# Kernel optimization log

Measured on AMD Instinct MI355X. Metric: run time of the kernel, lower is better.

The kernel has to match this reference:

```python
import jax, jax.numpy as jnp
import numpy as np

B, N = 4, 512
NZ = 95
BOX = 25.0                      # Angstrom box for random coords
CUTOFF = 15.0
SMOOTH_ON = 12.0                # cutoff * (1 - 0.2)
SMOOTH_OFF = 15.0
A1, A2, S6, S8 = 0.4145, 4.8593, 1.0, 1.2177
K1, K3 = 16.0, 4.0              # standard DFT-D3 CN / gaussian-weight constants
BOHR = 1.8897261258369282       # Angstrom -> Bohr
H2EV = 27.211386245988          # Hartree -> eV


def setup_inputs() -> dict:
    key = jax.random.key(0)
    k = jax.random.split(key, 6)
    coord = jax.random.uniform(k[0], (B, N, 3), jnp.float32) * BOX
    numbers = jax.random.randint(k[1], (B, N), 0, 86).astype(jnp.int64)
    rcov = jax.random.uniform(k[2], (NZ,), jnp.float32) * 2.0 + 1.0      # Bohr
    r4r2 = jax.random.uniform(k[3], (NZ,), jnp.float32) * 3.0 + 2.0      # a.u.
    c6ab = jax.random.uniform(k[4], (NZ, NZ, 5, 5), jnp.float32) * 20.0 + 1.0
    cn_ref = jax.random.uniform(k[5], (NZ, NZ, 5, 5), jnp.float32) * 4.0
    return dict(coord=coord, numbers=numbers, rcov=rcov, r4r2=r4r2,
                c6ab=c6ab, cn_ref=cn_ref)


def _d3_energy(coord, rcov, r4r2, c6ab, cn_ref, numbers):
    z = numbers
    # pairwise distances [B,N,N] (Angstrom), self-pairs masked
    diff = coord[:, :, None, :] - coord[:, None, :, :]
    r2 = (diff * diff).sum(-1)
    eye = jnp.eye(N, dtype=bool)[None]
    r2_safe = jnp.where(eye, 1.0, r2)
    r_ang = jnp.sqrt(r2_safe)
    pair_mask = (~eye) & (r_ang <= CUTOFF)
    r = r_ang * BOHR  # Bohr

    # coordination numbers: CN_i = sum_j 1/(1+exp(-k1*(rcov_ij/r - 1)))
    rc = rcov[z]                                   # [B,N]
    rco = rc[:, :, None] + rc[:, None, :]          # [B,N,N]
    cn_pair = jnp.where(pair_mask,
                        1.0 / (1.0 + jnp.exp(-K1 * (rco / r - 1.0))), 0.0)
    cn = cn_pair.sum(-1)                           # [B,N]

    # C6 interpolation over 5x5 reference-CN grid (gather-heavy)
    zi = z[:, :, None]   # [B,N,1]
    zj = z[:, None, :]   # [B,1,N]
    c6_ref = c6ab[zi, zj]                               # [B,N,N,5,5]
    cni_ref = cn_ref[zi, zj]                            # ref CN of atom i
    cnj_ref = jnp.swapaxes(cn_ref[zj, zi], -1, -2)      # ref CN of atom j
    dcn_i = cn[:, :, None, None, None] - cni_ref
    dcn_j = cn[:, None, :, None, None] - cnj_ref
    w = jnp.where(c6_ref > 0.0,
                  jnp.exp(-K3 * (dcn_i * dcn_i + dcn_j * dcn_j)), 0.0)
    wsum = w.sum((-1, -2))
    c6 = (c6_ref * w).sum((-1, -2)) / (wsum + 1e-20)    # [B,N,N]

    # C8 and BJ damping radius
    rr = r4r2[z]
    r4r2ij = rr[:, :, None] * rr[:, None, :]
    c8 = 3.0 * c6 * r4r2ij
    r0 = jnp.sqrt(3.0 * r4r2ij)     # sqrt(C8/C6)
    f = A1 * r0 + A2

    r6 = r2_safe * BOHR * BOHR
    r6 = r6 * r6 * r6               # r^6 in Bohr
    r8 = r6 * r * r
    e_pair = S6 * c6 / (r6 + f ** 6) + S8 * c8 / (r8 + f ** 8)

    # cutoff smoothing (smoothstep from SMOOTH_ON to SMOOTH_OFF, in Angstrom)
    x = jnp.clip((r_ang - SMOOTH_ON) / (SMOOTH_OFF - SMOOTH_ON), 0.0, 1.0)
    sw = 1.0 - x * x * (3.0 - 2.0 * x)
    e_pair = jnp.where(pair_mask, e_pair * sw, 0.0)

    # each pair counted twice in the dense matrix -> 0.5 factor; Hartree->eV
    return -0.5 * e_pair.sum((1, 2)) * H2EV   # [B]


def reference(coord, numbers, rcov, r4r2, c6ab, cn_ref):
    return _d3_energy(coord, rcov, r4r2, c6ab, cn_ref, numbers)
```

## Files before the change

kernel.cpp:

```cpp
#include <hip/hip_runtime.h>

#define NA   512
#define NB   4
#define NZT  95

#define FUSED_ELEMS (NZT * NZT * 25)
#define FUSED_BYTES (FUSED_ELEMS * 16)
#define FUSE_BLOCKS ((FUSED_ELEMS + 255) / 256)

#define SORT_OFF (((FUSED_BYTES + 63) / 64) * 64)
#define ARR_B    (NB * NA * 4)
#define EBLOCKS  (NB * NA * NA / 256)

__global__ void __launch_bounds__(256) prep_kernel(
    const float* __restrict__ coord,
    const int*   __restrict__ numbers,
    const float* __restrict__ rcov,
    const float* __restrict__ r4r2,
    const float* __restrict__ c6ab,
    const float* __restrict__ cn_ref,
    float4*      __restrict__ fused,
    float*       __restrict__ xs,
    float*       __restrict__ ys,
    float*       __restrict__ zs,
    float*       __restrict__ rcs,
    float*       __restrict__ rrs,
    int*         __restrict__ zsp)
{
    const int blk = blockIdx.x;
    if (blk < NB) {
        const int b = blk;
        __shared__ int hist[NZT];
        __shared__ int offs[NZT];
        for (int t = threadIdx.x; t < NZT; t += 256) hist[t] = 0;
        __syncthreads();

        const int i0 = threadIdx.x;
        const int i1 = threadIdx.x + 256;
        const int z0 = numbers[b * NA + i0];
        const int z1 = numbers[b * NA + i1];
        atomicAdd(&hist[z0], 1);
        atomicAdd(&hist[z1], 1);
        __syncthreads();
        if (threadIdx.x == 0) {
            int s = 0;
            for (int k = 0; k < NZT; ++k) { offs[k] = s; s += hist[k]; }
        }
        __syncthreads();

        const float* cb = coord + (size_t)b * NA * 3;
        const int base = b * NA;

        const int p0 = base + atomicAdd(&offs[z0], 1);
        xs[p0]  = cb[3 * i0 + 0];
        ys[p0]  = cb[3 * i0 + 1];
        zs[p0]  = cb[3 * i0 + 2];
        rcs[p0] = rcov[z0];
        rrs[p0] = r4r2[z0];
        zsp[p0] = z0;

        const int p1 = base + atomicAdd(&offs[z1], 1);
        xs[p1]  = cb[3 * i1 + 0];
        ys[p1]  = cb[3 * i1 + 1];
        zs[p1]  = cb[3 * i1 + 2];
        rcs[p1] = rcov[z1];
        rrs[p1] = r4r2[z1];
        zsp[p1] = z1;
        return;
    }

    const int idx = (blk - NB) * 256 + threadIdx.x;
    if (idx >= FUSED_ELEMS) return;
    const int pair = idx / 25;
    const int k    = idx - pair * 25;
    const int a    = k / 5;
    const int b2   = k - a * 5;
    const int zi   = pair / NZT;
    const int zj   = pair - zi * NZT;

    const float c6 = c6ab[(size_t)pair * 25 + k];
    const float ci = cn_ref[(size_t)pair * 25 + k];
    const float cj = cn_ref[((size_t)zj * NZT + zi) * 25 + b2 * 5 + a];
    fused[idx] = make_float4(c6, ci, cj, 0.0f);
}

__global__ void __launch_bounds__(256) cn_kernel(
    const float* __restrict__ xs,
    const float* __restrict__ ys,
    const float* __restrict__ zs,
    const float* __restrict__ rcs,
    float*       __restrict__ cn)
{
    const int bi   = blockIdx.x;
    const int b    = bi >> 9;
    const int i    = bi & (NA - 1);
    const int base = b * NA;

    const float xi  = xs[base + i];
    const float yi  = ys[base + i];
    const float zi  = zs[base + i];
    const float rci = rcs[base + i];

    float acc = 0.0f;
    #pragma unroll
    for (int t = 0; t < 2; ++t) {
        const int j = threadIdx.x + t * 256;
        if (j == i) continue;
        const float dx = xi - xs[base + j];
        const float dy = yi - ys[base + j];
        const float dz = zi - zs[base + j];
        const float r2 = dx * dx + dy * dy + dz * dz;
        const float r_ang = sqrtf(r2);
        if (r_ang <= 15.0f) {
            const float rb  = r_ang * 1.8897261258369282f;
            const float rco = rci + rcs[base + j];
            acc += 1.0f / (1.0f + __expf(-16.0f * (rco / rb - 1.0f)));
        }
    }
    #pragma unroll
    for (int off = 32; off > 0; off >>= 1)
        acc += __shfl_down(acc, off, 64);

    __shared__ float red[4];
    const int wave = threadIdx.x >> 6;
    if ((threadIdx.x & 63) == 0) red[wave] = acc;
    __syncthreads();
    if (threadIdx.x == 0) cn[bi] = red[0] + red[1] + red[2] + red[3];
}

__global__ void __launch_bounds__(256) energy_kernel(
    const float*  __restrict__ xs,
    const float*  __restrict__ ys,
    const float*  __restrict__ zs,
    const float*  __restrict__ rrs,
    const int*    __restrict__ zsp,
    const float4* __restrict__ fused,
    const float*  __restrict__ cn,
    float*        __restrict__ partials)
{
    const int tid  = blockIdx.x * 256 + threadIdx.x;
    const int b    = tid >> 18;
    const int rem  = tid & (NA * NA - 1);
    const int i    = rem >> 9;
    const int j    = rem & (NA - 1);
    const int base = b * NA;

    float e = 0.0f;
    if (i != j) {
        const float dx = xs[base + i] - xs[base + j];
        const float dy = ys[base + i] - ys[base + j];
        const float dz = zs[base + i] - zs[base + j];
        const float r2 = dx * dx + dy * dy + dz * dz;
        const float r_ang = sqrtf(r2);
        if (r_ang <= 15.0f) {
            const int zi = __builtin_amdgcn_readfirstlane(zsp[base + i]);
            const int zj = zsp[base + j];
            const float cni = cn[base + i];
            const float cnj = cn[base + j];

            const float4* tp = fused + ((size_t)zi * NZT + zj) * 25;

            float wsum = 0.0f, c6w = 0.0f;
            #pragma unroll
            for (int k = 0; k < 25; ++k) {
                const float4 t = tp[k];
                const float di = cni - t.y;
                const float dj = cnj - t.z;
                float s = di * di;
                s = fmaf(dj, dj, s);
                float w = __expf(-4.0f * s);
                w = (t.x > 0.0f) ? w : 0.0f;
                wsum += w;
                c6w  = fmaf(t.x, w, c6w);
            }
            const float c6 = c6w / (wsum + 1e-20f);

            const float rrij = rrs[base + i] * rrs[base + j];
            const float c8   = 3.0f * c6 * rrij;
            const float r0   = sqrtf(3.0f * rrij);
            const float f    = 0.4145f * r0 + 4.8593f;

            const float B2  = 1.8897261258369282f * 1.8897261258369282f;
            const float r2b = r2 * B2;
            const float r6  = r2b * r2b * r2b;
            const float r8  = r6 * r2b;
            const float f2  = f * f;
            const float f6  = f2 * f2 * f2;
            const float f8  = f6 * f2;

            float ep = c6 / (r6 + f6) + 1.2177f * c8 / (r8 + f8);

            float x = (r_ang - 12.0f) * (1.0f / 3.0f);
            x = fminf(fmaxf(x, 0.0f), 1.0f);
            const float sw = 1.0f - x * x * (3.0f - 2.0f * x);
            e = ep * sw;
        }
    }

    #pragma unroll
    for (int off = 32; off > 0; off >>= 1)
        e += __shfl_down(e, off, 64);

    __shared__ float red[4];
    const int wave = threadIdx.x >> 6;
    if ((threadIdx.x & 63) == 0) red[wave] = e;
    __syncthreads();
    if (threadIdx.x == 0)
        partials[blockIdx.x] = red[0] + red[1] + red[2] + red[3];
}

__global__ void __launch_bounds__(256) reduce_kernel(
    const float* __restrict__ partials,
    float*       __restrict__ out)
{
    const int b = blockIdx.x;
    const int P = EBLOCKS / NB;
    float s = 0.0f;
    #pragma unroll
    for (int t = 0; t < P / 256; ++t)
        s += partials[b * P + threadIdx.x + t * 256];

    #pragma unroll
    for (int off = 32; off > 0; off >>= 1)
        s += __shfl_down(s, off, 64);

    __shared__ float red[4];
    const int wave = threadIdx.x >> 6;
    if ((threadIdx.x & 63) == 0) red[wave] = s;
    __syncthreads();
    if (threadIdx.x == 0) {
        const float tot = red[0] + red[1] + red[2] + red[3];
        out[b] = tot * (-0.5f * 27.211386245988f);
    }
}

extern "C" void kernel_launch(void* const* d_in, const int* in_sizes, int n_in,
                              void* d_out, int out_size, void* d_ws, size_t ws_size,
                              hipStream_t stream) {
    const float* coord   = (const float*)d_in[0];
    const int*   numbers = (const int*)  d_in[1];
    const float* rcov    = (const float*)d_in[2];
    const float* r4r2    = (const float*)d_in[3];
    const float* c6ab    = (const float*)d_in[4];
    const float* cn_ref  = (const float*)d_in[5];
    float* out = (float*)d_out;

    char* ws = (char*)d_ws;
    float4* fused = (float4*)ws;
    float*  xs   = (float*)(ws + SORT_OFF + 0 * ARR_B);
    float*  ys   = (float*)(ws + SORT_OFF + 1 * ARR_B);
    float*  zs   = (float*)(ws + SORT_OFF + 2 * ARR_B);
    float*  rcs  = (float*)(ws + SORT_OFF + 3 * ARR_B);
    float*  rrs  = (float*)(ws + SORT_OFF + 4 * ARR_B);
    int*    zsp  = (int*)  (ws + SORT_OFF + 5 * ARR_B);
    float*  cn   = (float*)(ws + SORT_OFF + 6 * ARR_B);
    float*  part = (float*)(ws + SORT_OFF + 7 * ARR_B);

    prep_kernel<<<NB + FUSE_BLOCKS, 256, 0, stream>>>(
        coord, numbers, rcov, r4r2, c6ab, cn_ref,
        fused, xs, ys, zs, rcs, rrs, zsp);

    cn_kernel<<<NB * NA, 256, 0, stream>>>(xs, ys, zs, rcs, cn);

    energy_kernel<<<EBLOCKS, 256, 0, stream>>>(xs, ys, zs, rrs, zsp,
                                               fused, cn, part);

    reduce_kernel<<<NB, 256, 0, stream>>>(part, out);
}
```

Measured before the change: 90.33 us.

## Stage per-row C6 reference slice in LDS, one block per atom i

Energy kernel now assigns one block per (batch, atom i), with each thread handling two j atoms. The block loads the 95x25 float4 reference slice for element zi into shared memory, so the 25-entry table reads come from LDS instead of scattered global gathers. Per-i values are hoisted into scalars. This adds about 38KB of LDS per block, which limits occupancy, plus a per-block slice load. The partials count also changes, and the reduce kernel is assumed to use EBLOCKS consistently.

```diff
diff --git a/kernel.cpp b/kernel.cpp
--- a/kernel.cpp
+++ b/kernel.cpp
@@ -7,10 +7,11 @@
 #define FUSED_ELEMS (NZT * NZT * 25)
 #define FUSED_BYTES (FUSED_ELEMS * 16)
 #define FUSE_BLOCKS ((FUSED_ELEMS + 255) / 256)
+#define SLICE      (NZT * 25)
 
 #define SORT_OFF (((FUSED_BYTES + 63) / 64) * 64)
 #define ARR_B    (NB * NA * 4)
-#define EBLOCKS  (NB * NA * NA / 256)
+#define EBLOCKS  (NB * NA)
 
 __global__ void __launch_bounds__(256) prep_kernel(
     const float* __restrict__ coord,
@@ -138,44 +139,57 @@
     const float*  __restrict__ cn,
     float*        __restrict__ partials)
 {
-    const int tid  = blockIdx.x * 256 + threadIdx.x;
-    const int b    = tid >> 18;
-    const int rem  = tid & (NA * NA - 1);
-    const int i    = rem >> 9;
-    const int j    = rem & (NA - 1);
+    const int blk  = blockIdx.x;
+    const int b    = blk >> 9;
+    const int i    = blk & (NA - 1);
     const int base = b * NA;
 
+    __shared__ float4 tile[SLICE];
+
+    const int zi = zsp[base + i];
+    const float4* src = fused + (size_t)zi * SLICE;
+    for (int t = threadIdx.x; t < SLICE; t += 256)
+        tile[t] = src[t];
+
+    const float xi  = xs[base + i];
+    const float yi  = ys[base + i];
+    const float zci = zs[base + i];
+    const float cni = cn[base + i];
+    const float rri = rrs[base + i];
+    __syncthreads();
+
     float e = 0.0f;
-    if (i != j) {
-        const float dx = xs[base + i] - xs[base + j];
-        const float dy = ys[base + i] - ys[base + j];
-        const float dz = zs[base + i] - zs[base + j];
+    #pragma unroll
+    for (int t = 0; t < 2; ++t) {
+        const int j = threadIdx.x + t * 256;
+        if (j == i) continue;
+        const float dx = xi - xs[base + j];
+        const float dy = yi - ys[base + j];
+        const float dz = zci - zs[base + j];
         const float r2 = dx * dx + dy * dy + dz * dz;
         const float r_ang = sqrtf(r2);
         if (r_ang <= 15.0f) {
-            const int zi = __builtin_amdgcn_readfirstlane(zsp[base + i]);
             const int zj = zsp[base + j];
-            const float cni = cn[base + i];
             const float cnj = cn[base + j];
 
-            const float4* tp = fused + ((size_t)zi * NZT + zj) * 25;
+            const float4* tp = &tile[zj * 25];
 
             float wsum = 0.0f, c6w = 0.0f;
             #pragma unroll
             for (int k = 0; k < 25; ++k) {
-                const float4 t = tp[k];
-                const float di = cni - t.y;
-                const float dj = cnj - t.z;
+                const float4 tv = tp[k];
+                const float di = cni - tv.y;
+                const float dj = cnj - tv.z;
                 float s = di * di;
                 s = fmaf(dj, dj, s);
                 float w = __expf(-4.0f * s);
-                w = (t.x > 0.0f) ? w : 0.0f;
+                w = (tv.x > 0.0f) ? w : 0.0f;
                 wsum += w;
-                c6w  = fmaf(t.x, w, c6w);
+                c6w  = fmaf(tv.x, w, c6w);
             }
             const float c6 = c6w / (wsum + 1e-20f);
 
-            const float rrij = rrs[base + i] * rrs[base + j];
+            const float rrij = rri * rrs[base + j];
             const float c8   = 3.0f * c6 * rrij;
             const float r0   = sqrtf(3.0f * rrij);
             const float f    = 0.4145f * r0 + 4.8593f;
@@ -193,7 +207,7 @@
             float x = (r_ang - 12.0f) * (1.0f / 3.0f);
             x = fminf(fmaxf(x, 0.0f), 1.0f);
             const float sw = 1.0f - x * x * (3.0f - 2.0f * x);
-            e = ep * sw;
+            e = fmaf(ep, sw, e);
         }
     }
 
@@ -206,7 +220,7 @@
     if ((threadIdx.x & 63) == 0) red[wave] = e;
     __syncthreads();
     if (threadIdx.x == 0)
-        partials[blockIdx.x] = red[0] + red[1] + red[2] + red[3];
+        partials[blk] = red[0] + red[1] + red[2] + red[3];
 }
 
 __global__ void __launch_bounds__(256) reduce_kernel(
```

Result: slower. 92.49 us (+2.4%).
